# Performance work log

Measured on AMD Instinct MI355X. Metric: run time of the kernel, lower is better.

Reference implementation:

```python
import jax, jax.numpy as jnp
import numpy as np
import math

B, L, T, IN, H, DEPTH, HEADS = 4096, 1, 64, 16, 128, 3, 2
HD = H // HEADS
EPS = 1e-5


def layer_norm(x, g, b):
    u = jnp.mean(x, axis=-1, keepdims=True)
    s = jnp.mean((x - u) ** 2, axis=-1, keepdims=True)
    return g * (x - u) / jnp.sqrt(s + EPS) + b


def mlp(x, W, b, g, beta):
    return jax.nn.relu(layer_norm(x @ W + b, g, beta))


def attention(h, amask, Wq, bq, Wk, bk, Wv, bv):
    N, Tn, _ = h.shape
    def heads(x):
        return x.reshape(N, Tn, HEADS, HD).transpose(0, 2, 1, 3)
    q = heads(h @ Wq + bq)
    k = heads(h @ Wk + bk)
    v = heads(h @ Wv + bv)
    scores = jnp.einsum('nhqd,nhkd->nhqk', q, k) / math.sqrt(HD)
    scores = scores + (1.0 - amask[:, None]) * -10000.0
    probs = jax.nn.softmax(scores, axis=-1)
    ctx = jnp.einsum('nhqk,nhkd->nhqd', probs, v)
    return ctx.transpose(0, 2, 1, 3).reshape(N, Tn, H)


def setup_inputs() -> dict:
    key = jax.random.key(0)
    ks = jax.random.split(key, 8)
    feat = jax.random.normal(ks[0], (B, L, T, IN), jnp.float32)
    seq_lens = jax.random.randint(ks[1], (B, L), 1, T + 1)
    pos = jnp.arange(T)
    # repo convention: 0 = valid node, 1 = padded; prefix-valid layout
    masks = (pos[None, None, :] >= seq_lens[..., None]).astype(jnp.float32)[..., None]
    s = 0.02
    W_emb = jax.random.normal(ks[2], (IN, H), jnp.float32) * s
    W_enc = jax.random.normal(ks[3], (H, H), jnp.float32) * s
    Wq = jax.random.normal(ks[4], (DEPTH, H, H), jnp.float32) * s
    Wk = jax.random.normal(ks[5], (DEPTH, H, H), jnp.float32) * s
    Wv = jax.random.normal(ks[6], (DEPTH, H, H), jnp.float32) * s
    return dict(
        lane_nodes_feat=feat, masks=masks,
        W_emb=W_emb, b_emb=jnp.zeros((H,)), g_emb=jnp.ones((H,)), beta_emb=jnp.zeros((H,)),
        W_enc=W_enc, b_enc=jnp.zeros((H,)), g_enc=jnp.ones((H,)), beta_enc=jnp.zeros((H,)),
        Wq=Wq, bq=jnp.zeros((DEPTH, H)), Wk=Wk, bk=jnp.zeros((DEPTH, H)), Wv=Wv, bv=jnp.zeros((DEPTH, H)),
        ln_g=jnp.ones((DEPTH, H)), ln_b=jnp.zeros((DEPTH, H)),
    )


def reference(lane_nodes_feat, masks, W_emb, b_emb, g_emb, beta_emb, W_enc, b_enc,
              g_enc, beta_enc, Wq, bq, Wk, bk, Wv, bv, ln_g, ln_b):
    emb = mlp(lane_nodes_feat, W_emb, b_emb, g_emb, beta_emb)   # [B,L,T,H]
    emb = mlp(emb, W_enc, b_enc, g_enc, beta_enc)
    # every (b,l) lane has >=1 valid node by construction, so masked_select == reshape
    hs = emb.reshape(B * L, T, H)
    seq_lens = jnp.sum(1.0 - masks[:, :, :, 0], axis=-1).reshape(B * L)  # [N]
    pos = jnp.arange(T)
    valid = pos[None, :] < seq_lens[:, None]                              # [N,T]
    amask = (valid[:, :, None] & valid[:, None, :]).astype(hs.dtype)      # [N,T,T]
    for d in range(DEPTH):
        temp = hs
        hs = attention(hs, amask, Wq[d], bq[d], Wk[d], bk[d], Wv[d], bv[d])
        hs = jax.nn.relu(hs) + temp
        hs = layer_norm(hs, ln_g[d], ln_b[d])
    hs = jnp.max(hs, axis=1)                                              # [N,H]
    return hs.reshape(B, L, H)
```

## Files before the change

### kernel.cpp

```cpp
#include <hip/hip_runtime.h>

typedef unsigned short u16;
typedef unsigned int u32;
typedef __attribute__((ext_vector_type(8))) short short8_;
typedef short8_ short8 __attribute__((may_alias));
typedef uint2 uint2a __attribute__((may_alias));
typedef uint4 uint4a __attribute__((may_alias));
typedef ushort4 ushort4a __attribute__((may_alias));
typedef float4 float4a __attribute__((may_alias));
typedef __attribute__((ext_vector_type(4))) float floatx4;

#define EPSV 1e-5f
#define WS_ELEMS 167936
#define LOG2E 1.442695040888963f

__device__ __forceinline__ float b2f(u16 u){
  union { float f; u32 i; } c; c.i = ((u32)u) << 16; return c.f;
}
__device__ __forceinline__ u16 f2b(float f){
  union { float f; u32 i; } c; c.f = f;
  u32 r = c.i + 0x7FFFu + ((c.i >> 16) & 1u);
  return (u16)(r >> 16);
}
__device__ __forceinline__ u32 pkbf(float lo, float hi){
  u32 r; asm("v_cvt_pk_bf16_f32 %0, %1, %2" : "=v"(r) : "v"(lo), "v"(hi));
  return r;
}
__device__ __forceinline__ float ldf(const void* p, int i, bool isf){
  return isf ? ((const float*)p)[i] : b2f(((const u16*)p)[i]);
}
__device__ __forceinline__ float4 ldf4(const void* p, int i4, bool isf){
  if (isf) return ((const float4a*)p)[i4];
  ushort4 u = ((const ushort4a*)p)[i4];
  return make_float4(b2f(u.x), b2f(u.y), b2f(u.z), b2f(u.w));
}
__device__ __forceinline__ bool detect_f32(const void* g_emb){
  return *(const u32*)g_emb == 0x3F800000u;
}
__device__ __forceinline__ void dma16(const u16* g, u16* l){
  __builtin_amdgcn_global_load_lds((const __attribute__((address_space(1))) u32*)(g),
                                   (__attribute__((address_space(3))) u32*)(l), 16, 0, 0);
}
__device__ __forceinline__ void dma_slab(const u16* g, u16* dst, int wave, int lane){
  #pragma unroll
  for (int i = 0; i < 4; i++){
    int c = (wave << 2) + i;
    dma16(g + (c << 9) + (lane << 3), dst + (c << 9));
  }
}

__global__ void prep_kernel(const void* W_emb, const void* W_enc,
                            const void* Wq, const void* Wk, const void* Wv,
                            const void* g_emb, u16* ws){
  bool isf = detect_f32(g_emb);
  int e = blockIdx.x * 256 + threadIdx.x;
  if (e >= WS_ELEMS) return;
  float v;
  if (e < 4096){
    int half = e >> 11, r = e & 2047;
    int nt = r >> 9, q = (r >> 3) & 63, j = r & 7;
    int col = half*64 + nt*16 + (q & 15);
    int k = (q >> 4)*8 + j;
    v = (k < 16) ? ldf(W_emb, k*128 + col, isf) : 0.0f;
  } else if (e < 20480){
    int i = e - 4096;
    int half = i >> 13, r = i & 8191;
    int chunk = r >> 9, q = (r >> 3) & 63, j = r & 7;
    int ks = chunk >> 2, nt = chunk & 3;
    int col = half*64 + nt*16 + (q & 15);
    int k = ks*32 + (q >> 4)*8 + j;
    v = ldf(W_enc, k*128 + col, isf);
  } else {
    int i = e - 20480;
    int slab = i >> 13, r = i & 8191;
    int dh = slab / 3, which = slab - dh*3;
    int d = dh >> 1, h = dh & 1;
    int chunk = r >> 9, q = (r >> 3) & 63, j = r & 7;
    int ks = chunk >> 2, nt = chunk & 3;
    int col = h*64 + nt*16 + (q & 15);
    int k = ks*32 + (q >> 4)*8 + j;
    const void* W = (which == 0) ? Wv : (which == 1) ? Wk : Wq;
    v = ldf(W, d*16384 + k*128 + col, isf);
  }
  ws[e] = f2b(v);
}

__device__ __forceinline__ short8 frg(const u16* p, int chunk, int lane){
  return *(const short8*)(p + (chunk << 9) + (lane << 3));
}
__device__ __forceinline__ void wr4(u16* dst, int off, float v0, float v1, float v2, float v3){
  uint2 w; w.x = pkbf(v0, v1); w.y = pkbf(v2, v3);
  *(uint2a*)(dst + off) = w;
}
__device__ __forceinline__ int toff(int wave, int nt, int lq, int lc){
  return ((((nt >> 1) << 2) + wave) << 9)
       + ((((((nt & 1) << 1) + (lq >> 1)) << 4) + lc) << 3) + ((lq & 1) << 2);
}
__device__ __forceinline__ int voff(int wave, int nt, int lq, int lc){
  return ((((wave >> 1) << 2) + nt) << 9)
       + ((((((wave & 1) << 1) + (lq >> 1)) << 4) + lc) << 3) + ((lq & 1) << 2);
}
__device__ __forceinline__ int qoff(int wave, int nt, int lq, int lc){
  return (wave << 10) + ((nt >> 1) << 9)
       + ((((((nt & 1) << 1) + (lq >> 1)) << 4) + lc) << 3) + ((lq & 1) << 2);
}

__device__ __forceinline__ void gemmW(const u16* sh, const u16* slab, int wave, int lane, floatx4* acc){
  #pragma unroll
  for (int ks = 0; ks < 4; ks++){
    short8 a = frg(sh, ks*4 + wave, lane);
    #pragma unroll
    for (int nt = 0; nt < 4; nt++)
      acc[nt] = __builtin_amdgcn_mfma_f32_16x16x32_bf16(a, frg(slab, ks*4 + nt, lane), acc[nt], 0, 0, 0);
  }
}
__device__ __forceinline__ void gemmT(const u16* slab, const u16* sh, int wave, int lane, floatx4* acc){
  #pragma unroll
  for (int ks = 0; ks < 4; ks++){
    short8 b = frg(sh, ks*4 + wave, lane);
    #pragma unroll
    for (int nt = 0; nt < 4; nt++)
      acc[nt] = __builtin_amdgcn_mfma_f32_16x16x32_bf16(frg(slab, ks*4 + nt, lane), b, acc[nt], 0, 0, 0);
  }
}

__device__ __forceinline__ void ln_mlp_T(floatx4* acc, const void* bias, const void* g,
    const void* bet, bool isf, int wave, int lq, int lc, u16* sh){
  float x[8][4]; float s1 = 0.0f, s2 = 0.0f;
  #pragma unroll
  for (int nt = 0; nt < 8; nt++){
    float4 bb = ldf4(bias, nt*4 + lq, isf);
    float v0 = acc[nt][0] + bb.x, v1 = acc[nt][1] + bb.y;
    float v2 = acc[nt][2] + bb.z, v3 = acc[nt][3] + bb.w;
    x[nt][0]=v0; x[nt][1]=v1; x[nt][2]=v2; x[nt][3]=v3;
    s1 += (v0+v1) + (v2+v3);
    s2 += (v0*v0+v1*v1) + (v2*v2+v3*v3);
  }
  s1 += __shfl_xor(s1, 16, 64); s2 += __shfl_xor(s2, 16, 64);
  s1 += __shfl_xor(s1, 32, 64); s2 += __shfl_xor(s2, 32, 64);
  float mean = s1 * (1.0f/128.0f);
  float rstd = rsqrtf(s2*(1.0f/128.0f) - mean*mean + EPSV);
  #pragma unroll
  for (int nt = 0; nt < 8; nt++){
    float4 gg = ldf4(g, nt*4 + lq, isf), bb = ldf4(bet, nt*4 + lq, isf);
    float y0 = fmaxf((x[nt][0]-mean)*rstd*gg.x + bb.x, 0.0f);
    float y1 = fmaxf((x[nt][1]-mean)*rstd*gg.y + bb.y, 0.0f);
    float y2 = fmaxf((x[nt][2]-mean)*rstd*gg.z + bb.z, 0.0f);
    float y3 = fmaxf((x[nt][3]-mean)*rstd*gg.w + bb.w, 0.0f);
    wr4(sh, toff(wave, nt, lq, lc), y0, y1, y2, y3);
  }
}

__device__ __forceinline__ void ln_attn_T_res(floatx4* ctx, const u16* cb,
                                              int wave, int lq, int lc, u16* sh){
  float x[8][4]; float s1 = 0.0f, s2 = 0.0f;
  #pragma unroll
  for (int nt = 0; nt < 8; nt++){
    ushort4 rs = *(const ushort4a*)(sh + toff(wave, nt, lq, lc));
    float v0 = fmaxf(ctx[nt][0], 0.0f) + b2f(rs.x);
    float v1 = fmaxf(ctx[nt][1], 0.0f) + b2f(rs.y);
    float v2 = fmaxf(ctx[nt][2], 0.0f) + b2f(rs.z);
    float v3 = fmaxf(ctx[nt][3], 0.0f) + b2f(rs.w);
    x[nt][0]=v0; x[nt][1]=v1; x[nt][2]=v2; x[nt][3]=v3;
    s1 += (v0+v1) + (v2+v3);
    s2 += (v0*v0+v1*v1) + (v2*v2+v3*v3);
  }
  s1 += __shfl_xor(s1, 16, 64); s2 += __shfl_xor(s2, 16, 64);
  s1 += __shfl_xor(s1, 32, 64); s2 += __shfl_xor(s2, 32, 64);
  float mean = s1 * (1.0f/128.0f);
  float rstd = rsqrtf(s2*(1.0f/128.0f) - mean*mean + EPSV);
  #pragma unroll
  for (int nt = 0; nt < 8; nt++){
    ushort4 g4 = *(const ushort4a*)(cb + 384 + nt*16 + lq*4);
    ushort4 b4 = *(const ushort4a*)(cb + 512 + nt*16 + lq*4);
    float y0 = (x[nt][0]-mean)*rstd*b2f(g4.x) + b2f(b4.x);
    float y1 = (x[nt][1]-mean)*rstd*b2f(g4.y) + b2f(b4.y);
    float y2 = (x[nt][2]-mean)*rstd*b2f(g4.z) + b2f(b4.z);
    float y3 = (x[nt][3]-mean)*rstd*b2f(g4.w) + b2f(b4.w);
    wr4(sh, toff(wave, nt, lq, lc), y0, y1, y2, y3);
  }
}

__global__ __launch_bounds__(256, 3)
void fused_kernel(const void* feat, const void* masks,
                  const void* b_emb, const void* g_emb, const void* be_emb,
                  const void* b_enc, const void* g_enc, const void* be_enc,
                  const void* bq, const void* bk, const void* bv,
                  const void* ln_g, const void* ln_b,
                  const u16* ws, void* out){
  __shared__ __align__(16) u16 s_h[8192];
  __shared__ __align__(16) u16 s_w[8192];
  __shared__ __align__(16) u16 s_k[4096];
  __shared__ __align__(16) u16 s_v[4096];
  __shared__ __align__(16) u16 s_c[1920];
  __shared__ __align__(16) float s_valid[64];

  int tid = threadIdx.x;
  int wave = tid >> 6, lane = tid & 63, lq = lane >> 4, lc = lane & 15;
  int n = blockIdx.x;
  bool isf = detect_f32(g_emb);
  const floatx4 z4 = {0.0f, 0.0f, 0.0f, 0.0f};

  dma16(ws + ((wave*2 + 0) << 9) + (lane << 3), s_w + ((wave*2 + 0) << 9));
  dma16(ws + ((wave*2 + 1) << 9) + (lane << 3), s_w + ((wave*2 + 1) << 9));

  if (!isf){
    const u16* fp = (const u16*)feat + n*1024;
    if (tid < 128){
      int t = tid >> 1, half = tid & 1;
      uint4 v = *(const uint4a*)(fp + t*16 + half*8);
      *(uint4a*)(s_h + ((t >> 4) << 9) + (((half << 4) + (t & 15)) << 3)) = v;
    } else {
      int t = (tid - 128) >> 1, half = 2 + ((tid - 128) & 1);
      uint4 z; z.x = 0; z.y = 0; z.z = 0; z.w = 0;
      *(uint4a*)(s_h + ((t >> 4) << 9) + (((half << 4) + (t & 15)) << 3)) = z;
    }
  } else {
    for (int i = tid; i < 2048; i += 256){
      int t = i >> 5, k = i & 31;
      float v = (k < 16) ? ((const float*)feat)[n*1024 + t*16 + k] : 0.0f;
      s_h[((t >> 4) << 9) + ((((k >> 3) << 4) + (t & 15)) << 3) + (k & 7)] = f2b(v);
    }
  }
  for (int i = tid; i < 1920; i += 256){
    int blk = i >> 7, off = i & 127;
    int d = blk / 5, wh = blk - d*5;
    const void* src = (wh == 0) ? bq : (wh == 1) ? bk : (wh == 2) ? bv : (wh == 3) ? ln_g : ln_b;
    s_c[i] = isf ? f2b(((const float*)src)[d*128 + off]) : ((const u16*)src)[d*128 + off];
  }
  if (tid < 64) s_valid[tid] = (ldf(masks, n*64 + tid, isf) == 0.0f) ? 1.0f : 0.0f;
  __syncthreads();

  float madd[4][4];
  {
    float vq = s_valid[wave*16 + lc];
    #pragma unroll
    for (int nt = 0; nt < 4; nt++){
      float4 v4 = *(const float4a*)&s_valid[nt*16 + lq*4];
      madd[nt][0] = (10000.0f*vq*v4.x - 10000.0f) * LOG2E;
      madd[nt][1] = (10000.0f*vq*v4.y - 10000.0f) * LOG2E;
      madd[nt][2] = (10000.0f*vq*v4.z - 10000.0f) * LOG2E;
      madd[nt][3] = (10000.0f*vq*v4.w - 10000.0f) * LOG2E;
    }
  }

  floatx4 acc[8];
  #pragma unroll
  for (int i = 0; i < 8; i++) acc[i] = z4;
  {
    short8 b = frg(s_h, wave, lane);
    #pragma unroll
    for (int nt = 0; nt < 8; nt++)
      acc[nt] = __builtin_amdgcn_mfma_f32_16x16x32_bf16(frg(s_w, nt, lane), b, acc[nt], 0, 0, 0);
  }
  __syncthreads();
  dma_slab(ws + 4096, s_w, wave, lane);
  ln_mlp_T(acc, b_emb, g_emb, be_emb, isf, wave, lq, lc, s_h);
  __syncthreads();

  #pragma unroll
  for (int i = 0; i < 8; i++) acc[i] = z4;
  gemmT(s_w, s_h, wave, lane, acc);
  __syncthreads();
  dma_slab(ws + 12288, s_w, wave, lane);
  __syncthreads();
  gemmT(s_w, s_h, wave, lane, acc + 4);
  __syncthreads();
  dma_slab(ws + 20480, s_w, wave, lane);
  ln_mlp_T(acc, b_enc, g_enc, be_enc, isf, wave, lq, lc, s_h);
  __syncthreads();

  int sb = 20480;
  for (int d = 0; d < 3; d++){
    const u16* cb = s_c + d*640;
    floatx4 ctx[8];
    #pragma unroll
    for (int i = 0; i < 8; i++) ctx[i] = z4;

    #pragma unroll
    for (int h = 0; h < 2; h++){
      floatx4 pa[4];
      bool last = (d == 2 && h == 1);
      #pragma unroll
      for (int i = 0; i < 4; i++) pa[i] = z4;
      gemmW(s_h, s_w, wave, lane, pa);
      __syncthreads();
      dma_slab(ws + sb + 8192, s_w, wave, lane);
      #pragma unroll
      for (int nt = 0; nt < 4; nt++){
        float bb = b2f(cb[256 + h*64 + nt*16 + lc]);
        wr4(s_v, voff(wave, nt, lq, lc),
            pa[nt][0]+bb, pa[nt][1]+bb, pa[nt][2]+bb, pa[nt][3]+bb);
      }
      __syncthreads();
      #pragma unroll
      for (int i = 0; i < 4; i++) pa[i] = z4;
      gemmT(s_w, s_h, wave, lane, pa);
      __syncthreads();
      dma_slab(ws + sb + 16384, s_w, wave, lane);
      #pragma unroll
      for (int nt = 0; nt < 4; nt++){
        ushort4 b4 = *(const ushort4a*)(cb + 128 + h*64 + nt*16 + lq*4);
        wr4(s_k, toff(wave, nt, lq, lc),
            pa[nt][0]+b2f(b4.x), pa[nt][1]+b2f(b4.y),
            pa[nt][2]+b2f(b4.z), pa[nt][3]+b2f(b4.w));
      }
      __syncthreads();
      #pragma unroll
      for (int i = 0; i < 4; i++) pa[i] = z4;
      gemmT(s_w, s_h, wave, lane, pa);
      __syncthreads();
      if (!last && wave >= 2) dma_slab(ws + sb + 24576, s_w, wave, lane);
      #pragma unroll
      for (int nt = 0; nt < 4; nt++){
        ushort4 b4 = *(const ushort4a*)(cb + h*64 + nt*16 + lq*4);
        wr4(s_w, qoff(wave, nt, lq, lc),
            pa[nt][0]+b2f(b4.x), pa[nt][1]+b2f(b4.y),
            pa[nt][2]+b2f(b4.z), pa[nt][3]+b2f(b4.w));
      }
      #pragma unroll
      for (int i = 0; i < 4; i++) pa[i] = z4;
      {
        const u16* qp = s_w + (wave << 10);
        #pragma unroll
        for (int ks = 0; ks < 2; ks++){
          short8 b = *(const short8*)(qp + (ks << 9) + (lane << 3));
          #pragma unroll
          for (int nt = 0; nt < 4; nt++)
            pa[nt] = __builtin_amdgcn_mfma_f32_16x16x32_bf16(frg(s_k, ks*4 + nt, lane), b, pa[nt], 0, 0, 0);
        }
      }
      {
        float p[4][4];
        #pragma unroll
        for (int nt = 0; nt < 4; nt++)
          #pragma unroll
          for (int r = 0; r < 4; r++)
            p[nt][r] = fmaf(pa[nt][r], 0.125f*LOG2E, madd[nt][r]);
        float m0 = fmaxf(fmaxf(p[0][0],p[0][1]), fmaxf(p[0][2],p[0][3]));
        float m1 = fmaxf(fmaxf(p[1][0],p[1][1]), fmaxf(p[1][2],p[1][3]));
        float m2 = fmaxf(fmaxf(p[2][0],p[2][1]), fmaxf(p[2][2],p[2][3]));
        float m3 = fmaxf(fmaxf(p[3][0],p[3][1]), fmaxf(p[3][2],p[3][3]));
        float mx = fmaxf(fmaxf(m0,m1), fmaxf(m2,m3));
        mx = fmaxf(mx, __shfl_xor(mx, 16, 64));
        mx = fmaxf(mx, __shfl_xor(mx, 32, 64));
        float sm = 0.0f;
        #pragma unroll
        for (int nt = 0; nt < 4; nt++)
          #pragma unroll
          for (int r = 0; r < 4; r++){
            p[nt][r] = __builtin_amdgcn_exp2f(p[nt][r] - mx);
            sm += p[nt][r];
          }
        sm += __shfl_xor(sm, 16, 64);
        sm += __shfl_xor(sm, 32, 64);
        float inv = 1.0f / sm;
        #pragma unroll
        for (int nt = 0; nt < 4; nt++)
          wr4(s_w, qoff(wave, nt, lq, lc),
              p[nt][0]*inv, p[nt][1]*inv, p[nt][2]*inv, p[nt][3]*inv);
      }
      {
        const u16* qp = s_w + (wave << 10);
        #pragma unroll
        for (int ks = 0; ks < 2; ks++){
          short8 b = *(const short8*)(qp + (ks << 9) + (lane << 3));
          #pragma unroll
          for (int nt = 0; nt < 4; nt++)
            ctx[h*4+nt] = __builtin_amdgcn_mfma_f32_16x16x32_bf16(frg(s_v, ks*4 + nt, lane), b, ctx[h*4+nt], 0, 0, 0);
        }
      }
      __syncthreads();
      sb += 24576;
      if (!last && wave < 2) dma_slab(ws + sb, s_w, wave, lane);
      if (h == 1) ln_attn_T_res(ctx, cb, wave, lq, lc, s_h);
      __syncthreads();
    }
  }

  {
    int col = tid >> 1, th = tid & 1;
    int base = ((col >> 5) << 2);
    int lp = (((col >> 3) & 3) << 4);
    int jj = col & 7;
    float mxv = -1e30f;
    #pragma unroll 8
    for (int t = 0; t < 32; t++){
      int tt = (th << 5) + t;
      mxv = fmaxf(mxv, b2f(s_h[((base + (tt >> 4)) << 9) + ((lp + (tt & 15)) << 3) + jj]));
    }
    mxv = fmaxf(mxv, __shfl_xor(mxv, 1, 64));
    if (!th){
      if (isf) ((float*)out)[n*128 + col] = mxv;
      else     ((u16*)out)[n*128 + col]  = f2b(mxv);
    }
  }
}

extern "C" void kernel_launch(void* const* d_in, const int* in_sizes, int n_in,
                              void* d_out, int out_size, void* d_ws, size_t ws_size,
                              hipStream_t stream){
  const void* feat   = d_in[0];
  const void* masks  = d_in[1];
  const void* W_emb  = d_in[2];
  const void* b_emb  = d_in[3];
  const void* g_emb  = d_in[4];
  const void* be_emb = d_in[5];
  const void* W_enc  = d_in[6];
  const void* b_enc  = d_in[7];
  const void* g_enc  = d_in[8];
  const void* be_enc = d_in[9];
  const void* Wq     = d_in[10];
  const void* bq     = d_in[11];
  const void* Wk     = d_in[12];
  const void* bk     = d_in[13];
  const void* Wv     = d_in[14];
  const void* bv     = d_in[15];
  const void* ln_g   = d_in[16];
  const void* ln_b   = d_in[17];
  u16* ws = (u16*)d_ws;

  hipLaunchKernelGGL(prep_kernel, dim3((WS_ELEMS + 255)/256), dim3(256), 0, stream,
                     W_emb, W_enc, Wq, Wk, Wv, g_emb, ws);
  hipLaunchKernelGGL(fused_kernel, dim3(4096), dim3(256), 0, stream,
                     feat, masks, b_emb, g_emb, be_emb, b_enc, g_enc, be_enc,
                     bq, bk, bv, ln_g, ln_b, ws, d_out);
}
```

Measured before the change: 333.3 us.

## Double-buffer weight slabs in LDS to overlap loads with GEMMs

Doubles the shared weight buffer into two slabs and ping-pongs between them, so the next weight slab is prefetched while the current GEMM runs. This removes several __syncthreads barriers and exposed weight-load latency in the MLP and attention phases, and factors each attention head into a helper. The extra 16 KB of LDS lowers the launch bound from 3 to 2 blocks per CU, which reduces occupancy and latency hiding across blocks.

```diff
diff --git a/kernel.cpp b/kernel.cpp
--- a/kernel.cpp
+++ b/kernel.cpp
@@ -181,7 +181,98 @@
   }
 }
 
-__global__ __launch_bounds__(256, 3)
+__device__ __forceinline__ void attn_phase(
+    const u16* ws_sb, u16* Wv, u16* Wsc, const u16* s_h, u16* s_k, u16* s_v,
+    const u16* cb, int h, const float madd[4][4], floatx4* ctxh,
+    int wave, int lane, int lq, int lc, bool last)
+{
+  const floatx4 z4 = {0.0f, 0.0f, 0.0f, 0.0f};
+  floatx4 pa[4];
+  dma_slab(ws_sb + 8192, Wsc, wave, lane);
+  #pragma unroll
+  for (int i = 0; i < 4; i++) pa[i] = z4;
+  gemmW(s_h, Wv, wave, lane, pa);
+  #pragma unroll
+  for (int nt = 0; nt < 4; nt++){
+    float bb = b2f(cb[256 + h*64 + nt*16 + lc]);
+    wr4(s_v, voff(wave, nt, lq, lc),
+        pa[nt][0]+bb, pa[nt][1]+bb, pa[nt][2]+bb, pa[nt][3]+bb);
+  }
+  __syncthreads();
+  dma_slab(ws_sb + 16384, Wv, wave, lane);
+  #pragma unroll
+  for (int i = 0; i < 4; i++) pa[i] = z4;
+  gemmT(Wsc, s_h, wave, lane, pa);
+  #pragma unroll
+  for (int nt = 0; nt < 4; nt++){
+    ushort4 b4 = *(const ushort4a*)(cb + 128 + h*64 + nt*16 + lq*4);
+    wr4(s_k, toff(wave, nt, lq, lc),
+        pa[nt][0]+b2f(b4.x), pa[nt][1]+b2f(b4.y),
+        pa[nt][2]+b2f(b4.z), pa[nt][3]+b2f(b4.w));
+  }
+  __syncthreads();
+  if (!last) dma_slab(ws_sb + 24576, Wsc, wave, lane);
+  #pragma unroll
+  for (int i = 0; i < 4; i++) pa[i] = z4;
+  gemmT(Wv, s_h, wave, lane, pa);
+  __syncthreads();
+  #pragma unroll
+  for (int nt = 0; nt < 4; nt++){
+    ushort4 b4 = *(const ushort4a*)(cb + h*64 + nt*16 + lq*4);
+    wr4(Wv, qoff(wave, nt, lq, lc),
+        pa[nt][0]+b2f(b4.x), pa[nt][1]+b2f(b4.y),
+        pa[nt][2]+b2f(b4.z), pa[nt][3]+b2f(b4.w));
+  }
+  #pragma unroll
+  for (int i = 0; i < 4; i++) pa[i] = z4;
+  const u16* qp = Wv + (wave << 10);
+  #pragma unroll
+  for (int ks = 0; ks < 2; ks++){
+    short8 b = *(const short8*)(qp + (ks << 9) + (lane << 3));
+    #pragma unroll
+    for (int nt = 0; nt < 4; nt++)
+      pa[nt] = __builtin_amdgcn_mfma_f32_16x16x32_bf16(frg(s_k, ks*4 + nt, lane), b, pa[nt], 0, 0, 0);
+  }
+  {
+    float p[4][4];
+    #pragma unroll
+    for (int nt = 0; nt < 4; nt++)
+      #pragma unroll
+      for (int r = 0; r < 4; r++)
+        p[nt][r] = fmaf(pa[nt][r], 0.125f*LOG2E, madd[nt][r]);
+    float m0 = fmaxf(fmaxf(p[0][0],p[0][1]), fmaxf(p[0][2],p[0][3]));
+    float m1 = fmaxf(fmaxf(p[1][0],p[1][1]), fmaxf(p[1][2],p[1][3]));
+    float m2 = fmaxf(fmaxf(p[2][0],p[2][1]), fmaxf(p[2][2],p[2][3]));
+    float m3 = fmaxf(fmaxf(p[3][0],p[3][1]), fmaxf(p[3][2],p[3][3]));
+    float mx = fmaxf(fmaxf(m0,m1), fmaxf(m2,m3));
+    mx = fmaxf(mx, __shfl_xor(mx, 16, 64));
+    mx = fmaxf(mx, __shfl_xor(mx, 32, 64));
+    float sm = 0.0f;
+    #pragma unroll
+    for (int nt = 0; nt < 4; nt++)
+      #pragma unroll
+      for (int r = 0; r < 4; r++){
+        p[nt][r] = __builtin_amdgcn_exp2f(p[nt][r] - mx);
+        sm += p[nt][r];
+      }
+    sm += __shfl_xor(sm, 16, 64);
+    sm += __shfl_xor(sm, 32, 64);
+    float inv = 1.0f / sm;
+    #pragma unroll
+    for (int nt = 0; nt < 4; nt++)
+      wr4(Wv, qoff(wave, nt, lq, lc),
+          p[nt][0]*inv, p[nt][1]*inv, p[nt][2]*inv, p[nt][3]*inv);
+  }
+  #pragma unroll
+  for (int ks = 0; ks < 2; ks++){
+    short8 b = *(const short8*)(qp + (ks << 9) + (lane << 3));
+    #pragma unroll
+    for (int nt = 0; nt < 4; nt++)
+      ctxh[nt] = __builtin_amdgcn_mfma_f32_16x16x32_bf16(frg(s_v, ks*4 + nt, lane), b, ctxh[nt], 0, 0, 0);
+  }
+}
+
+__global__ __launch_bounds__(256, 2)
 void fused_kernel(const void* feat, const void* masks,
                   const void* b_emb, const void* g_emb, const void* be_emb,
                   const void* b_enc, const void* g_enc, const void* be_enc,
@@ -189,11 +280,14 @@
                   const void* ln_g, const void* ln_b,
                   const u16* ws, void* out){
   __shared__ __align__(16) u16 s_h[8192];
-  __shared__ __align__(16) u16 s_w[8192];
+  __shared__ __align__(16) u16 s_w[16384];
   __shared__ __align__(16) u16 s_k[4096];
   __shared__ __align__(16) u16 s_v[4096];
   __shared__ __align__(16) u16 s_c[1920];
   __shared__ __align__(16) float s_valid[64];
+
+  u16* W0 = s_w;
+  u16* W1 = s_w + 8192;
 
   int tid = threadIdx.x;
   int wave = tid >> 6, lane = tid & 63, lq = lane >> 4, lc = lane & 15;
@@ -201,8 +295,9 @@
   bool isf = detect_f32(g_emb);
   const floatx4 z4 = {0.0f, 0.0f, 0.0f, 0.0f};
 
-  dma16(ws + ((wave*2 + 0) << 9) + (lane << 3), s_w + ((wave*2 + 0) << 9));
-  dma16(ws + ((wave*2 + 1) << 9) + (lane << 3), s_w + ((wave*2 + 1) << 9));
+  dma16(ws + ((wave*2 + 0) << 9) + (lane << 3), W0 + ((wave*2 + 0) << 9));
+  dma16(ws + ((wave*2 + 1) << 9) + (lane << 3), W0 + ((wave*2 + 1) << 9));
+  dma_slab(ws + 4096, W1, wave, lane);
 
   if (!isf){
     const u16* fp = (const u16*)feat + n*1024;
@@ -251,22 +346,17 @@
     short8 b = frg(s_h, wave, lane);
     #pragma unroll
     for (int nt = 0; nt < 8; nt++)
-      acc[nt] = __builtin_amdgcn_mfma_f32_16x16x32_bf16(frg(s_w, nt, lane), b, acc[nt], 0, 0, 0);
-  }
-  __syncthreads();
-  dma_slab(ws + 4096, s_w, wave, lane);
+      acc[nt] = __builtin_amdgcn_mfma_f32_16x16x32_bf16(frg(W0, nt, lane), b, acc[nt], 0, 0, 0);
+  }
+  __syncthreads();
+  dma_slab(ws + 12288, W0, wave, lane);
   ln_mlp_T(acc, b_emb, g_emb, be_emb, isf, wave, lq, lc, s_h);
-  __syncthreads();
-
   #pragma unroll
   for (int i = 0; i < 8; i++) acc[i] = z4;
-  gemmT(s_w, s_h, wave, lane, acc);
-  __syncthreads();
-  dma_slab(ws + 12288, s_w, wave, lane);
-  __syncthreads();
-  gemmT(s_w, s_h, wave, lane, acc + 4);
-  __syncthreads();
-  dma_slab(ws + 20480, s_w, wave, lane);
+  gemmT(W1, s_h, wave, lane, acc);
+  __syncthreads();
+  dma_slab(ws + 20480, W1, wave, lane);
+  gemmT(W0, s_h, wave, lane, acc + 4);
   ln_mlp_T(acc, b_enc, g_enc, be_enc, isf, wave, lq, lc, s_h);
   __syncthreads();
 
@@ -277,105 +367,14 @@
     #pragma unroll
     for (int i = 0; i < 8; i++) ctx[i] = z4;
 
-    #pragma unroll
-    for (int h = 0; h < 2; h++){
-      floatx4 pa[4];
-      bool last = (d == 2 && h == 1);
-      #pragma unroll
-      for (int i = 0; i < 4; i++) pa[i] = z4;
-      gemmW(s_h, s_w, wave, lane, pa);
-      __syncthreads();
-      dma_slab(ws + sb + 8192, s_w, wave, lane);
-      #pragma unroll
-      for (int nt = 0; nt < 4; nt++){
-        float bb = b2f(cb[256 + h*64 + nt*16 + lc]);
-        wr4(s_v, voff(wave, nt, lq, lc),
-            pa[nt][0]+bb, pa[nt][1]+bb, pa[nt][2]+bb, pa[nt][3]+bb);
-      }
-      __syncthreads();
-      #pragma unroll
-      for (int i = 0; i < 4; i++) pa[i] = z4;
-      gemmT(s_w, s_h, wave, lane, pa);
-      __syncthreads();
-      dma_slab(ws + sb + 16384, s_w, wave, lane);
-      #pragma unroll
-      for (int nt = 0; nt < 4; nt++){
-        ushort4 b4 = *(const ushort4a*)(cb + 128 + h*64 + nt*16 + lq*4);
-        wr4(s_k, toff(wave, nt, lq, lc),
-            pa[nt][0]+b2f(b4.x), pa[nt][1]+b2f(b4.y),
-            pa[nt][2]+b2f(b4.z), pa[nt][3]+b2f(b4.w));
-      }
-      __syncthreads();
-      #pragma unroll
-      for (int i = 0; i < 4; i++) pa[i] = z4;
-      gemmT(s_w, s_h, wave, lane, pa);
-      __syncthreads();
-      if (!last && wave >= 2) dma_slab(ws + sb + 24576, s_w, wave, lane);
-      #pragma unroll
-      for (int nt = 0; nt < 4; nt++){
-        ushort4 b4 = *(const ushort4a*)(cb + h*64 + nt*16 + lq*4);
-        wr4(s_w, qoff(wave, nt, lq, lc),
-            pa[nt][0]+b2f(b4.x), pa[nt][1]+b2f(b4.y),
-            pa[nt][2]+b2f(b4.z), pa[nt][3]+b2f(b4.w));
-      }
-      #pragma unroll
-      for (int i = 0; i < 4; i++) pa[i] = z4;
-      {
-        const u16* qp = s_w + (wave << 10);
-        #pragma unroll
-        for (int ks = 0; ks < 2; ks++){
-          short8 b = *(const short8*)(qp + (ks << 9) + (lane << 3));
-          #pragma unroll
-          for (int nt = 0; nt < 4; nt++)
-            pa[nt] = __builtin_amdgcn_mfma_f32_16x16x32_bf16(frg(s_k, ks*4 + nt, lane), b, pa[nt], 0, 0, 0);
-        }
-      }
-      {
-        float p[4][4];
-        #pragma unroll
-        for (int nt = 0; nt < 4; nt++)
-          #pragma unroll
-          for (int r = 0; r < 4; r++)
-            p[nt][r] = fmaf(pa[nt][r], 0.125f*LOG2E, madd[nt][r]);
-        float m0 = fmaxf(fmaxf(p[0][0],p[0][1]), fmaxf(p[0][2],p[0][3]));
-        float m1 = fmaxf(fmaxf(p[1][0],p[1][1]), fmaxf(p[1][2],p[1][3]));
-        float m2 = fmaxf(fmaxf(p[2][0],p[2][1]), fmaxf(p[2][2],p[2][3]));
-        float m3 = fmaxf(fmaxf(p[3][0],p[3][1]), fmaxf(p[3][2],p[3][3]));
-        float mx = fmaxf(fmaxf(m0,m1), fmaxf(m2,m3));
-        mx = fmaxf(mx, __shfl_xor(mx, 16, 64));
-        mx = fmaxf(mx, __shfl_xor(mx, 32, 64));
-        float sm = 0.0f;
-        #pragma unroll
-        for (int nt = 0; nt < 4; nt++)
-          #pragma unroll
-          for (int r = 0; r < 4; r++){
-            p[nt][r] = __builtin_amdgcn_exp2f(p[nt][r] - mx);
-            sm += p[nt][r];
-          }
-        sm += __shfl_xor(sm, 16, 64);
-        sm += __shfl_xor(sm, 32, 64);
-        float inv = 1.0f / sm;
-        #pragma unroll
-        for (int nt = 0; nt < 4; nt++)
-          wr4(s_w, qoff(wave, nt, lq, lc),
-              p[nt][0]*inv, p[nt][1]*inv, p[nt][2]*inv, p[nt][3]*inv);
-      }
-      {
-        const u16* qp = s_w + (wave << 10);
-        #pragma unroll
-        for (int ks = 0; ks < 2; ks++){
-          short8 b = *(const short8*)(qp + (ks << 9) + (lane << 3));
-          #pragma unroll
-          for (int nt = 0; nt < 4; nt++)
-            ctx[h*4+nt] = __builtin_amdgcn_mfma_f32_16x16x32_bf16(frg(s_v, ks*4 + nt, lane), b, ctx[h*4+nt], 0, 0, 0);
-        }
-      }
-      __syncthreads();
-      sb += 24576;
-      if (!last && wave < 2) dma_slab(ws + sb, s_w, wave, lane);
-      if (h == 1) ln_attn_T_res(ctx, cb, wave, lq, lc, s_h);
-      __syncthreads();
-    }
+    attn_phase(ws + sb, W1, W0, s_h, s_k, s_v, cb, 0, madd, ctx + 0,
+               wave, lane, lq, lc, false);
+    __syncthreads();
+    attn_phase(ws + sb + 24576, W0, W1, s_h, s_k, s_v, cb, 1, madd, ctx + 4,
+               wave, lane, lq, lc, (d == 2));
+    ln_attn_T_res(ctx, cb, wave, lq, lc, s_h);
+    __syncthreads();
+    sb += 49152;
   }
 
   {
```

Result: slower. 395.1 us (+18.6%).
